# Kernel tuning notes

Measured on AMD Instinct MI355X. Metric: run time of the kernel, lower is better.

The kernel has to match this reference:

```python
import jax, jax.numpy as jnp
import numpy as np

B, S, D = 2, 2048, 2048
NH, NKV, HD = 16, 4, 128
EPS = 1e-6


def rmsnorm(x, w, eps=EPS):
    # torch.nn.RMSNorm: x * rsqrt(mean(x^2) + eps) * weight
    ms = jnp.mean(jnp.square(x), axis=-1, keepdims=True)
    return x * jax.lax.rsqrt(ms + eps) * w


def apply_rotary_emb(x, freqs_cis):
    # x: (B, S, H, HD); freqs_cis: (S, HD//2, 2) -> pairwise complex rotation (gpt-fast style)
    xs = x.reshape(*x.shape[:-1], -1, 2)          # (B,S,H,HD//2,2)
    fc = freqs_cis[None, :, None, :, :]           # (1,S,1,HD//2,2)
    xr, xi = xs[..., 0], xs[..., 1]
    fr, fi = fc[..., 0], fc[..., 1]
    out = jnp.stack([xr * fr - xi * fi, xi * fr + xr * fi], axis=-1)
    return out.reshape(x.shape)


def setup_inputs() -> dict:
    key = jax.random.key(0)
    ks = jax.random.split(key, 4)
    x = jax.random.normal(ks[0], (B, S, D), dtype=jnp.float32)
    freqs_cis = jax.random.normal(ks[1], (S, HD // 2, 2), dtype=jnp.float32)
    wqkv = jax.random.normal(ks[2], ((NH + 2 * NKV) * HD, D), dtype=jnp.float32) * (D ** -0.5)
    wo = jax.random.normal(ks[3], (NH * HD, D), dtype=jnp.float32).T * ((NH * HD) ** -0.5)
    wo = jnp.asarray(wo)  # (D, NH*HD) torch layout (out,in)
    q_norm_w = jnp.ones((HD,), dtype=jnp.float32)
    k_norm_w = jnp.ones((HD,), dtype=jnp.float32)
    return {"x": x, "freqs_cis": freqs_cis, "wqkv": wqkv, "wo": wo,
            "q_norm_w": q_norm_w, "k_norm_w": k_norm_w}


def reference(x, freqs_cis, wqkv, wo, q_norm_w, k_norm_w):
    b, s, _ = x.shape
    q_size, kv_size = NH * HD, NKV * HD
    qkv = jnp.einsum('bsd,ed->bse', x, wqkv)  # fused QKV projection
    q, k, v = jnp.split(qkv, [q_size, q_size + kv_size], axis=-1)
    q = q.reshape(b, s, NH, HD)
    k = k.reshape(b, s, NKV, HD)
    v = v.reshape(b, s, NKV, HD)
    q = rmsnorm(q, q_norm_w)
    k = rmsnorm(k, k_norm_w)
    q = apply_rotary_emb(q, freqs_cis)
    k = apply_rotary_emb(k, freqs_cis)
    # GQA: repeat_interleave KV heads to NH
    rep = NH // NKV
    k = jnp.repeat(k, rep, axis=2)  # (b,s,NH,HD)
    v = jnp.repeat(v, rep, axis=2)
    scale = 1.0 / np.sqrt(HD)
    scores = jnp.einsum('bqhd,bkhd->bhqk', q, k) * scale
    causal = jnp.tril(jnp.ones((s, s), dtype=bool))
    scores = jnp.where(causal[None, None], scores, -jnp.inf)
    attn = jax.nn.softmax(scores, axis=-1)
    y = jnp.einsum('bhqk,bkhd->bqhd', attn, v)
    y = y.reshape(b, s, q_size)
    return jnp.einsum('bse,de->bsd', y, wo)
```

## Files before the change

### kernel.cpp

```cpp
#include <hip/hip_runtime.h>
#include <math.h>

constexpr int B_ = 2, S_ = 2048, D_ = 2048, NH_ = 16, NKV_ = 4, HD_ = 128;
constexpr int EQKV_ = (NH_ + 2 * NKV_) * HD_;
constexpr int M_ = B_ * S_;
constexpr float EPS_ = 1e-6f;
constexpr float QSCALE_ = 0.08838834764831845f;

typedef __attribute__((ext_vector_type(8))) short bf16x8;
typedef __attribute__((ext_vector_type(4))) float f32x4;
typedef __attribute__((address_space(1))) unsigned int gu32;
typedef __attribute__((address_space(3))) unsigned int lu32;

__device__ inline ushort f2bf(float f) {
    unsigned u = __float_as_uint(f);
    return (ushort)((u + 0x7FFF + ((u >> 16) & 1)) >> 16);
}

constexpr int NP_X = M_ * D_ / 4;
constexpr int NP_W = EQKV_ * D_ / 4;
constexpr int NP_O = D_ * NH_ * HD_ / 4;
__global__ __launch_bounds__(256) void pack_all(
    const float* __restrict__ x, const float* __restrict__ wqkv,
    const float* __restrict__ wo,
    ushort* __restrict__ xbf, ushort* __restrict__ wqkvbf,
    ushort* __restrict__ wobf)
{
    int i = blockIdx.x * 256 + threadIdx.x;
    const float4* src; ushort4* dst; int j;
    if (i < NP_X)                 { src = (const float4*)x;    dst = (ushort4*)xbf;    j = i; }
    else if (i < NP_X + NP_W)     { src = (const float4*)wqkv; dst = (ushort4*)wqkvbf; j = i - NP_X; }
    else if (i < NP_X + NP_W + NP_O) { src = (const float4*)wo; dst = (ushort4*)wobf;  j = i - NP_X - NP_W; }
    else return;
    float4 f = src[j];
    ushort4 u;
    u.x = f2bf(f.x); u.y = f2bf(f.y); u.z = f2bf(f.z); u.w = f2bf(f.w);
    dst[j] = u;
}

__global__ __launch_bounds__(256) void gemm_nt_bf16(
    const ushort* __restrict__ A, const ushort* __restrict__ W,
    float* __restrict__ C, int M, int N, int K)
{
    __shared__ __align__(16) ushort As[128 * 64];
    __shared__ __align__(16) ushort Bs[128 * 64];
    const int t = threadIdx.x;
    const int wave = t >> 6, lane = t & 63;
    const int nwg = gridDim.x * gridDim.y;
    int wg = blockIdx.y * gridDim.x + blockIdx.x;
    wg = (wg & 7) * (nwg >> 3) + (wg >> 3);
    const int m0 = (wg / gridDim.x) * 128, n0 = (wg % gridDim.x) * 128;
    const int wm = (wave >> 1) * 64, wn = (wave & 1) * 64;
    const int lrow = lane & 15, lquad = lane >> 4;

    const int srow = t >> 3;
    const int sgo = ((t & 7) ^ (srow & 7)) * 8;
    const ushort* Aa = A + (size_t)(m0 + srow) * K + sgo;
    const ushort* Wa = W + (size_t)(n0 + srow) * K + sgo;
    const int rs0 = (lquad ^ (lrow & 7)) * 8;
    const int rs1 = rs0 ^ 32;

    f32x4 acc[4][4];
#pragma unroll
    for (int i = 0; i < 4; ++i)
#pragma unroll
        for (int j = 0; j < 4; ++j) acc[i][j] = (f32x4){0.f, 0.f, 0.f, 0.f};

    for (int k0 = 0; k0 < K; k0 += 64) {
        __syncthreads();
#pragma unroll
        for (int i = 0; i < 4; ++i) {
            const int ub = (wave * 64 + 256 * i) * 8;
            __builtin_amdgcn_global_load_lds(
                (const gu32*)(Aa + (size_t)(32 * i) * K + k0),
                (lu32*)(As + ub), 16, 0, 0);
            __builtin_amdgcn_global_load_lds(
                (const gu32*)(Wa + (size_t)(32 * i) * K + k0),
                (lu32*)(Bs + ub), 16, 0, 0);
        }
        __syncthreads();

#pragma unroll
        for (int ks = 0; ks < 2; ++ks) {
            const int so = ks ? rs1 : rs0;
            bf16x8 af[4], bf[4];
#pragma unroll
            for (int i = 0; i < 4; ++i) {
                af[i] = *(const bf16x8*)(As + (wm + i * 16 + lrow) * 64 + so);
                bf[i] = *(const bf16x8*)(Bs + (wn + i * 16 + lrow) * 64 + so);
            }
#pragma unroll
            for (int i = 0; i < 4; ++i)
#pragma unroll
                for (int j = 0; j < 4; ++j)
                    acc[i][j] = __builtin_amdgcn_mfma_f32_16x16x32_bf16(
                        af[i], bf[j], acc[i][j], 0, 0, 0);
        }
    }
#pragma unroll
    for (int i = 0; i < 4; ++i)
#pragma unroll
        for (int j = 0; j < 4; ++j) {
            float* cp = C + (size_t)(m0 + wm + i * 16 + lquad * 4) * N
                          + n0 + wn + j * 16 + lrow;
#pragma unroll
            for (int r = 0; r < 4; ++r) cp[(size_t)r * N] = acc[i][j][r];
        }
}

__global__ __launch_bounds__(256) void gemm_qkv_fused(
    const ushort* __restrict__ A,
    const ushort* __restrict__ W,
    const float* __restrict__ freqs,
    const float* __restrict__ qw, const float* __restrict__ kw,
    ushort* __restrict__ qo, ushort* __restrict__ ko, ushort* __restrict__ vo,
    int K)
{
    __shared__ __align__(16) ushort smem[128 * 136];
    __shared__ float rsbuf[256];
    ushort* As = smem;
    ushort* Bs = smem + 4096;
    ushort* Lt = smem;

    const int t = threadIdx.x;
    const int wave = t >> 6, lane = t & 63;
    const int nwg = gridDim.x * gridDim.y;
    int wg = blockIdx.y * gridDim.x + blockIdx.x;
    wg = (wg & 7) * (nwg >> 3) + (wg >> 3);
    const int m0 = (wg / gridDim.x) * 128, n0 = (wg % gridDim.x) * 128;
    const int wm = (wave >> 1) * 64, wn = (wave & 1) * 64;
    const int half = wave & 1;
    const int lrow = lane & 15, lquad = lane >> 4;
    const int head = n0 >> 7;
    const int b = m0 >> 11, s0 = m0 & (S_ - 1);

    f32x4 acc[4][4];
#pragma unroll
    for (int i = 0; i < 4; ++i)
#pragma unroll
        for (int j = 0; j < 4; ++j) acc[i][j] = (f32x4){0.f, 0.f, 0.f, 0.f};

    for (int k0 = 0; k0 < K; k0 += 32) {
        __syncthreads();
#pragma unroll
        for (int i = 0; i < 2; ++i) {
            int chunk = t + 256 * i;
            int row = chunk >> 2, seg = chunk & 3;
            int ubase = (wave * 64 + 256 * i) * 8;
            __builtin_amdgcn_global_load_lds(
                (const gu32*)(A + (size_t)(m0 + row) * K + k0 + seg * 8),
                (lu32*)(As + ubase), 16, 0, 0);
            __builtin_amdgcn_global_load_lds(
                (const gu32*)(W + (size_t)(n0 + row) * K + k0 + seg * 8),
                (lu32*)(Bs + ubase), 16, 0, 0);
        }
        __syncthreads();

        bf16x8 af[4], bf[4];
#pragma unroll
        for (int i = 0; i < 4; ++i) {
            af[i] = *(const bf16x8*)(As + (wm + i * 16 + lrow) * 32 + lquad * 8);
            bf[i] = *(const bf16x8*)(Bs + (wn + i * 16 + lrow) * 32 + lquad * 8);
        }
#pragma unroll
        for (int i = 0; i < 4; ++i)
#pragma unroll
            for (int j = 0; j < 4; ++j)
                acc[i][j] = __builtin_amdgcn_mfma_f32_16x16x32_bf16(
                    af[i], bf[j], acc[i][j], 0, 0, 0);
    }
    __syncthreads();

    float part[4][4];
    if (head < NH_ + NKV_) {
#pragma unroll
        for (int i = 0; i < 4; ++i)
#pragma unroll
            for (int r = 0; r < 4; ++r) {
                float p = acc[i][0][r] * acc[i][0][r]
                        + acc[i][1][r] * acc[i][1][r]
                        + acc[i][2][r] * acc[i][2][r]
                        + acc[i][3][r] * acc[i][3][r];
#pragma unroll
                for (int off = 1; off < 16; off <<= 1) p += __shfl_xor(p, off);
                part[i][r] = p;
                if (lrow == 0)
                    rsbuf[half * 128 + wm + i * 16 + lquad * 4 + r] = p;
            }
    }
    __syncthreads();

    if (head < NH_ + NKV_) {
        const float* nw = (head < NH_) ? qw : kw;
        float wv[4];
#pragma unroll
        for (int j = 0; j < 4; ++j) wv[j] = nw[wn + j * 16 + lrow];
#pragma unroll
        for (int i = 0; i < 4; ++i)
#pragma unroll
            for (int r = 0; r < 4; ++r) {
                const int rowid = wm + i * 16 + lquad * 4 + r;
                const int s = s0 + rowid;
                const float total = part[i][r] + rsbuf[(half ^ 1) * 128 + rowid];
                const float rs = rsqrtf(total * (1.0f / HD_) + EPS_);
#pragma unroll
                for (int j = 0; j < 4; ++j) {
                    const int d = wn + j * 16 + lrow;
                    const float xn = acc[i][j][r] * rs * wv[j];
                    const float other = __shfl_xor(xn, 1);
                    const float fr = freqs[s * HD_ + (d & ~1)];
                    const float fi = freqs[s * HD_ + (d & ~1) + 1];
                    float out = (d & 1) ? fmaf(xn, fr, other * fi)
                                        : fmaf(xn, fr, -other * fi);
                    if (head < NH_) out *= QSCALE_;
                    Lt[rowid * 136 + d] = f2bf(out);
                }
            }
    } else {
#pragma unroll
        for (int i = 0; i < 4; ++i)
#pragma unroll
            for (int j = 0; j < 4; ++j)
#pragma unroll
                for (int r = 0; r < 4; ++r)
                    Lt[(wn + j * 16 + lrow) * 136 + wm + i * 16 + lquad * 4 + r]
                        = f2bf(acc[i][j][r]);
    }
    __syncthreads();

    const int g = t >> 4, lx16 = t & 15;
    if (head < NH_) {
        ushort* dst0 = qo + ((size_t)(b * NH_ + head) * S_ + s0) * HD_;
#pragma unroll
        for (int it = 0; it < 8; ++it) {
            const int rowid = it * 16 + g;
            uint4 v = *(const uint4*)(Lt + rowid * 136 + lx16 * 8);
            *(uint4*)(dst0 + (size_t)rowid * HD_ + lx16 * 8) = v;
        }
    } else if (head < NH_ + NKV_) {
        const int kh = head - NH_;
        ushort* dst0 = ko + ((size_t)(b * NKV_ + kh) * S_ + s0) * HD_;
#pragma unroll
        for (int it = 0; it < 8; ++it) {
            const int rowid = it * 16 + g;
            uint4 v = *(const uint4*)(Lt + rowid * 136 + lx16 * 8);
            *(uint4*)(dst0 + (size_t)rowid * HD_ + lx16 * 8) = v;
        }
    } else {
        const int vh = head - (NH_ + NKV_);
        ushort* dst0 = vo + ((size_t)(b * NKV_ + vh) * HD_) * S_ + s0;
#pragma unroll
        for (int it = 0; it < 8; ++it) {
            const int rowid = it * 16 + g;
            uint4 v = *(const uint4*)(Lt + rowid * 136 + lx16 * 8);
            *(uint4*)(dst0 + (size_t)rowid * S_ + lx16 * 8) = v;
        }
    }
}

__global__ __launch_bounds__(512, 4) void flash_attn_mfma(
    const ushort* __restrict__ Q,
    const ushort* __restrict__ K,
    const ushort* __restrict__ V,
    ushort* __restrict__ Y,
    float* __restrict__ OP,
    float* __restrict__ ML)
{
    __shared__ __align__(16) ushort Ks[4 * 64 * 32];
    __shared__ __align__(16) ushort Vs[2 * 128 * 32];
    __shared__ __align__(16) ushort Ps[8 * 16 * 72];

    const int t = threadIdx.x, w = t >> 6, lane = t & 63;
    const int lx = lane & 15, quad = lane >> 4;
    const int h = blockIdx.y, b = blockIdx.z;

    const int gx = blockIdx.x;
    int qb, halfsel, tk0, tk1;
    bool split;
    if (gx < 22) {
        split = true;
        qb = 15 - (gx >> 1);
        halfsel = gx & 1;
        const int h0 = qb + 1;
        tk0 = halfsel ? h0 : 0;
        tk1 = halfsel ? 2 * qb + 2 : h0;
    } else {
        split = false;
        qb = 26 - gx;
        halfsel = 0;
        tk0 = 0;
        tk1 = 2 * qb + 2;
    }
    const int q0 = qb * 128;
    const int kvh = h >> 2;

    const int srow8 = lane >> 3, sseg8 = lane & 7;
    const int fsw = (srow8 >> 1) & 3;
    const int slotw = ((sseg8 & 3) ^ fsw) * 8;
    const int krow = w * 8 + srow8;
    const int d0 = w * 8 + srow8;
    ushort* kdst = Ks + (sseg8 >> 2) * 2048 + krow * 32 + slotw;
    ushort* vdst = Vs + (sseg8 >> 2) * 4096 + d0 * 32 + slotw;
    const ushort* ksrc = K + ((size_t)(b * NKV_ + kvh) * S_ + krow) * HD_
                           + sseg8 * 8;
    const ushort* vsrc = V + ((size_t)(b * NKV_ + kvh) * HD_ + d0) * S_
                           + sseg8 * 8;
    const int rslot = (quad ^ ((lx >> 1) & 3)) * 8;

    const ushort* qb_ = Q + ((size_t)(b * NH_ + h) * S_ + q0) * HD_;
    bf16x8 aq[4];
#pragma unroll
    for (int ks = 0; ks < 4; ++ks)
        aq[ks] = *(const bf16x8*)(qb_ + (size_t)(w * 16 + lx) * HD_ + ks * 32 + quad * 8);

    f32x4 o[8];
#pragma unroll
    for (int j = 0; j < 8; ++j) o[j] = (f32x4){0.f, 0.f, 0.f, 0.f};
    float mrow[4] = {-INFINITY, -INFINITY, -INFINITY, -INFINITY};
    float lp[4] = {0.f, 0.f, 0.f, 0.f};

    uint4 kr0, kr1, vr0, vr1;
    {
        const size_t kf = (size_t)tk0 * 64;
        kr0 = *(const uint4*)(ksrc + kf * HD_);
        kr1 = *(const uint4*)(ksrc + kf * HD_ + 64);
        vr0 = *(const uint4*)(vsrc + kf);
        vr1 = *(const uint4*)(vsrc + (size_t)64 * S_ + kf);
    }

    for (int tk = tk0; tk < tk1; ++tk) {
        const int k0 = tk * 64;
        asm volatile("s_barrier" ::: "memory");
        *(uint4*)(kdst +    0) = kr0;
        *(uint4*)(kdst + 4096) = kr1;
        *(uint4*)(vdst +    0) = vr0;
        *(uint4*)(vdst + 2048) = vr1;
        asm volatile("s_waitcnt lgkmcnt(0)" ::: "memory");
        asm volatile("s_barrier" ::: "memory");

        if (tk + 1 < tk1) {
            const size_t kf = (size_t)(k0 + 64);
            kr0 = *(const uint4*)(ksrc + kf * HD_);
            kr1 = *(const uint4*)(ksrc + kf * HD_ + 64);
            vr0 = *(const uint4*)(vsrc + kf);
            vr1 = *(const uint4*)(vsrc + (size_t)64 * S_ + kf);
        }

        f32x4 s[4];
#pragma unroll
        for (int j = 0; j < 4; ++j) s[j] = (f32x4){0.f, 0.f, 0.f, 0.f};
        __builtin_amdgcn_s_setprio(1);
#pragma unroll
        for (int ks = 0; ks < 4; ++ks) {
#pragma unroll
            for (int j = 0; j < 4; ++j) {
                bf16x8 bk = *(const bf16x8*)(Ks + ks * 2048 + (j * 16 + lx) * 32 + rslot);
                s[j] = __builtin_amdgcn_mfma_f32_16x16x32_bf16(aq[ks], bk, s[j], 0, 0, 0);
            }
        }
        __builtin_amdgcn_s_setprio(0);

        const int qrow_base = q0 + w * 16 + quad * 4;
        if (k0 + 63 > q0 + w * 16) {
#pragma unroll
            for (int reg = 0; reg < 4; ++reg) {
                const int qrow = qrow_base + reg;
#pragma unroll
                for (int j = 0; j < 4; ++j)
                    if (k0 + lx + 16 * j > qrow) s[j][reg] = -INFINITY;
            }
        }

        float rmx[4];
        bool need = false;
#pragma unroll
        for (int reg = 0; reg < 4; ++reg) {
            rmx[reg] = fmaxf(fmaxf(s[0][reg], s[1][reg]),
                             fmaxf(s[2][reg], s[3][reg]));
            need |= (rmx[reg] > mrow[reg] + 8.0f);
        }
        if (__any(need)) {
#pragma unroll
            for (int reg = 0; reg < 4; ++reg) {
                float rm = rmx[reg];
#pragma unroll
                for (int off = 1; off < 16; off <<= 1)
                    rm = fmaxf(rm, __shfl_xor(rm, off));
                const float mn = fmaxf(mrow[reg], rm);
                const float alpha = __expf(mrow[reg] - mn);
                mrow[reg] = mn;
                lp[reg] *= alpha;
#pragma unroll
                for (int j = 0; j < 8; ++j) o[j][reg] *= alpha;
            }
        }
#pragma unroll
        for (int reg = 0; reg < 4; ++reg) {
#pragma unroll
            for (int j = 0; j < 4; ++j) {
                const float p = __expf(s[j][reg] - mrow[reg]);
                lp[reg] += p;
                Ps[w * 1152 + (quad * 4 + reg) * 72 + lx + 16 * j] = f2bf(p);
            }
        }

        bf16x8 ap[2];
#pragma unroll
        for (int ks2 = 0; ks2 < 2; ++ks2)
            ap[ks2] = *(const bf16x8*)(Ps + w * 1152 + lx * 72 + ks2 * 32 + quad * 8);
        __builtin_amdgcn_s_setprio(1);
#pragma unroll
        for (int jd = 0; jd < 8; ++jd) {
#pragma unroll
            for (int ks2 = 0; ks2 < 2; ++ks2) {
                bf16x8 bv = *(const bf16x8*)(Vs + ks2 * 4096 + (jd * 16 + lx) * 32 + rslot);
                o[jd] = __builtin_amdgcn_mfma_f32_16x16x32_bf16(ap[ks2], bv, o[jd], 0, 0, 0);
            }
        }
        __builtin_amdgcn_s_setprio(0);
    }

#pragma unroll
    for (int reg = 0; reg < 4; ++reg) {
        float l = lp[reg];
#pragma unroll
        for (int off = 1; off < 16; off <<= 1) l += __shfl_xor(l, off);
        lp[reg] = l;
    }
    if (!split) {
#pragma unroll
        for (int reg = 0; reg < 4; ++reg) {
            const float inv = 1.0f / lp[reg];
            const size_t yb = (size_t)(b * S_ + q0 + w * 16 + quad * 4 + reg) * (NH_ * HD_)
                            + h * HD_ + lx;
#pragma unroll
            for (int jd = 0; jd < 8; ++jd)
                Y[yb + jd * 16] = f2bf(o[jd][reg] * inv);
        }
    } else {
        const int sp = ((b * NH_ + h) * 11 + (qb - 5)) * 2 + halfsel;
        float* mlb = ML + (size_t)sp * 256;
#pragma unroll
        for (int reg = 0; reg < 4; ++reg) {
            const int row = w * 16 + quad * 4 + reg;
            if (lx == 0) {
                mlb[row] = mrow[reg];
                mlb[128 + row] = lp[reg];
            }
            float* ob = OP + ((size_t)sp * 128 + row) * 128 + lx;
#pragma unroll
            for (int jd = 0; jd < 8; ++jd)
                ob[jd * 16] = o[jd][reg];
        }
    }
}

__global__ __launch_bounds__(256) void attn_combine(
    const float* __restrict__ OP, const float* __restrict__ ML,
    ushort* __restrict__ Y)
{
    const int gx = blockIdx.x, h = blockIdx.y, b = blockIdx.z;
    const int qb = 5 + gx;
    const int q0 = qb * 128;
    const int sp0 = ((b * NH_ + h) * 11 + gx) * 2;
    const float* ml0 = ML + (size_t)sp0 * 256;
    const float* ml1 = ML + (size_t)(sp0 + 1) * 256;
    const float* o0 = OP + (size_t)sp0 * 128 * 128;
    const float* o1 = OP + (size_t)(sp0 + 1) * 128 * 128;
    const int d = threadIdx.x & 127, rg = threadIdx.x >> 7;
#pragma unroll
    for (int r = rg; r < 128; r += 2) {
        const float m0 = ml0[r], l0 = ml0[128 + r];
        const float m1 = ml1[r], l1 = ml1[128 + r];
        const float m = fmaxf(m0, m1);
        const float w0 = __expf(m0 - m), w1 = __expf(m1 - m);
        const float inv = 1.0f / (l0 * w0 + l1 * w1);
        const float v = (o0[r * 128 + d] * w0 + o1[r * 128 + d] * w1) * inv;
        Y[((size_t)(b * S_ + q0 + r)) * (NH_ * HD_) + h * HD_ + d] = f2bf(v);
    }
}

extern "C" void kernel_launch(void* const* d_in, const int* in_sizes, int n_in,
                              void* d_out, int out_size, void* d_ws, size_t ws_size,
                              hipStream_t stream)
{
    const float* x     = (const float*)d_in[0];
    const float* freqs = (const float*)d_in[1];
    const float* wqkv  = (const float*)d_in[2];
    const float* wo    = (const float*)d_in[3];
    const float* qw    = (const float*)d_in[4];
    const float* kw    = (const float*)d_in[5];
    float* out = (float*)d_out;

    char* ws = (char*)d_ws;
    ushort* qbf    = (ushort*)(ws + 0);
    ushort* kbf    = (ushort*)(ws + 16777216);
    ushort* vtb    = (ushort*)(ws + 20971520);
    ushort* ybf    = (ushort*)(ws + 25165824);
    ushort* wobf   = (ushort*)(ws + 41943040);
    ushort* wqkvbf = (ushort*)(ws + 50331648);
    ushort* xbf    = (ushort*)(ws + 83886080);
    float*  OP     = (float*)(ws + 50331648);
    float*  ML     = (float*)(ws + 96468992);

    pack_all<<<(NP_X + NP_W + NP_O + 255) / 256, 256, 0, stream>>>(
        x, wqkv, wo, xbf, wqkvbf, wobf);
    gemm_qkv_fused<<<dim3(EQKV_ / 128, M_ / 128), 256, 0, stream>>>(
        xbf, wqkvbf, freqs, qw, kw, qbf, kbf, vtb, D_);
    flash_attn_mfma<<<dim3(27, NH_, B_), 512, 0, stream>>>(qbf, kbf, vtb, ybf,
                                                           OP, ML);
    attn_combine<<<dim3(11, NH_, B_), 256, 0, stream>>>(OP, ML, ybf);
    gemm_nt_bf16<<<dim3(D_ / 128, M_ / 128), 256, 0, stream>>>(
        ybf, wobf, out, M_, D_, NH_ * HD_);
}
```

Measured before the change: 335.9 us.

## Split QKV GEMM K-dimension across two wave groups with in-block reduction

```diff
diff --git a/kernel.cpp b/kernel.cpp
--- a/kernel.cpp
+++ b/kernel.cpp
@@ -108,7 +108,7 @@
         }
 }
 
-__global__ __launch_bounds__(256) void gemm_qkv_fused(
+__global__ __launch_bounds__(512, 4) void gemm_qkv_fused(
     const ushort* __restrict__ A,
     const ushort* __restrict__ W,
     const float* __restrict__ freqs,
@@ -116,51 +116,57 @@
     ushort* __restrict__ qo, ushort* __restrict__ ko, ushort* __restrict__ vo,
     int K)
 {
-    __shared__ __align__(16) ushort smem[128 * 136];
+    __shared__ __align__(16) ushort smem[17408];
     __shared__ float rsbuf[256];
-    ushort* As = smem;
-    ushort* Bs = smem + 4096;
     ushort* Lt = smem;
+    float* red = (float*)smem;
 
     const int t = threadIdx.x;
     const int wave = t >> 6, lane = t & 63;
+    const int grp = wave >> 2;
+    const int wl = wave & 3;
+    const int tl = t & 255;
     const int nwg = gridDim.x * gridDim.y;
     int wg = blockIdx.y * gridDim.x + blockIdx.x;
     wg = (wg & 7) * (nwg >> 3) + (wg >> 3);
     const int m0 = (wg / gridDim.x) * 128, n0 = (wg % gridDim.x) * 128;
-    const int wm = (wave >> 1) * 64, wn = (wave & 1) * 64;
-    const int half = wave & 1;
+    const int wm = (wl >> 1) * 64, wn = (wl & 1) * 64;
+    const int half = wl & 1;
     const int lrow = lane & 15, lquad = lane >> 4;
     const int head = n0 >> 7;
     const int b = m0 >> 11, s0 = m0 & (S_ - 1);
 
+    ushort* Ag = smem + grp * 4096;
+    ushort* Bg = smem + 8192 + grp * 4096;
+    const int kbase = grp * 1024;
+
     f32x4 acc[4][4];
 #pragma unroll
     for (int i = 0; i < 4; ++i)
 #pragma unroll
         for (int j = 0; j < 4; ++j) acc[i][j] = (f32x4){0.f, 0.f, 0.f, 0.f};
 
-    for (int k0 = 0; k0 < K; k0 += 32) {
+    for (int k0 = 0; k0 < 1024; k0 += 32) {
         __syncthreads();
 #pragma unroll
         for (int i = 0; i < 2; ++i) {
-            int chunk = t + 256 * i;
+            int chunk = tl + 256 * i;
             int row = chunk >> 2, seg = chunk & 3;
-            int ubase = (wave * 64 + 256 * i) * 8;
+            int ubase = (wl * 64 + 256 * i) * 8;
             __builtin_amdgcn_global_load_lds(
-                (const gu32*)(A + (size_t)(m0 + row) * K + k0 + seg * 8),
-                (lu32*)(As + ubase), 16, 0, 0);
+                (const gu32*)(A + (size_t)(m0 + row) * K + kbase + k0 + seg * 8),
+                (lu32*)(Ag + ubase), 16, 0, 0);
             __builtin_amdgcn_global_load_lds(
-                (const gu32*)(W + (size_t)(n0 + row) * K + k0 + seg * 8),
-                (lu32*)(Bs + ubase), 16, 0, 0);
+                (const gu32*)(W + (size_t)(n0 + row) * K + kbase + k0 + seg * 8),
+                (lu32*)(Bg + ubase), 16, 0, 0);
         }
         __syncthreads();
 
         bf16x8 af[4], bf[4];
 #pragma unroll
         for (int i = 0; i < 4; ++i) {
-            af[i] = *(const bf16x8*)(As + (wm + i * 16 + lrow) * 32 + lquad * 8);
-            bf[i] = *(const bf16x8*)(Bs + (wn + i * 16 + lrow) * 32 + lquad * 8);
+            af[i] = *(const bf16x8*)(Ag + (wm + i * 16 + lrow) * 32 + lquad * 8);
+            bf[i] = *(const bf16x8*)(Bg + (wn + i * 16 + lrow) * 32 + lquad * 8);
         }
 #pragma unroll
         for (int i = 0; i < 4; ++i)
@@ -169,10 +175,36 @@
                 acc[i][j] = __builtin_amdgcn_mfma_f32_16x16x32_bf16(
                     af[i], bf[j], acc[i][j], 0, 0, 0);
     }
+
     __syncthreads();
+#pragma unroll
+    for (int c = 0; c < 2; ++c) {
+        if (grp == 1 && half == c) {
+#pragma unroll
+            for (int i = 0; i < 4; ++i)
+#pragma unroll
+                for (int j = 0; j < 4; ++j)
+#pragma unroll
+                    for (int r = 0; r < 4; ++r)
+                        red[(wm + i * 16 + lquad * 4 + r) * 65 + j * 16 + lrow]
+                            = acc[i][j][r];
+        }
+        __syncthreads();
+        if (grp == 0 && half == c) {
+#pragma unroll
+            for (int i = 0; i < 4; ++i)
+#pragma unroll
+                for (int j = 0; j < 4; ++j)
+#pragma unroll
+                    for (int r = 0; r < 4; ++r)
+                        acc[i][j][r] +=
+                            red[(wm + i * 16 + lquad * 4 + r) * 65 + j * 16 + lrow];
+        }
+        __syncthreads();
+    }
 
     float part[4][4];
-    if (head < NH_ + NKV_) {
+    if (grp == 0 && head < NH_ + NKV_) {
 #pragma unroll
         for (int i = 0; i < 4; ++i)
 #pragma unroll
@@ -190,41 +222,43 @@
     }
     __syncthreads();
 
-    if (head < NH_ + NKV_) {
-        const float* nw = (head < NH_) ? qw : kw;
-        float wv[4];
-#pragma unroll
-        for (int j = 0; j < 4; ++j) wv[j] = nw[wn + j * 16 + lrow];
-#pragma unroll
-        for (int i = 0; i < 4; ++i)
-#pragma unroll
-            for (int r = 0; r < 4; ++r) {
-                const int rowid = wm + i * 16 + lquad * 4 + r;
-                const int s = s0 + rowid;
-                const float total = part[i][r] + rsbuf[(half ^ 1) * 128 + rowid];
-                const float rs = rsqrtf(total * (1.0f / HD_) + EPS_);
-#pragma unroll
-                for (int j = 0; j < 4; ++j) {
-                    const int d = wn + j * 16 + lrow;
-                    const float xn = acc[i][j][r] * rs * wv[j];
-                    const float other = __shfl_xor(xn, 1);
-                    const float fr = freqs[s * HD_ + (d & ~1)];
-                    const float fi = freqs[s * HD_ + (d & ~1) + 1];
-                    float out = (d & 1) ? fmaf(xn, fr, other * fi)
-                                        : fmaf(xn, fr, -other * fi);
-                    if (head < NH_) out *= QSCALE_;
-                    Lt[rowid * 136 + d] = f2bf(out);
+    if (grp == 0) {
+        if (head < NH_ + NKV_) {
+            const float* nw = (head < NH_) ? qw : kw;
+            float wv[4];
+#pragma unroll
+            for (int j = 0; j < 4; ++j) wv[j] = nw[wn + j * 16 + lrow];
+#pragma unroll
+            for (int i = 0; i < 4; ++i)
+#pragma unroll
+                for (int r = 0; r < 4; ++r) {
+                    const int rowid = wm + i * 16 + lquad * 4 + r;
+                    const int s = s0 + rowid;
+                    const float total = part[i][r] + rsbuf[(half ^ 1) * 128 + rowid];
+                    const float rs = rsqrtf(total * (1.0f / HD_) + EPS_);
+#pragma unroll
+                    for (int j = 0; j < 4; ++j) {
+                        const int d = wn + j * 16 + lrow;
+                        const float xn = acc[i][j][r] * rs * wv[j];
+                        const float other = __shfl_xor(xn, 1);
+                        const float fr = freqs[s * HD_ + (d & ~1)];
+                        const float fi = freqs[s * HD_ + (d & ~1) + 1];
+                        float out = (d & 1) ? fmaf(xn, fr, other * fi)
+                                            : fmaf(xn, fr, -other * fi);
+                        if (head < NH_) out *= QSCALE_;
+                        Lt[rowid * 136 + d] = f2bf(out);
+                    }
                 }
-            }
-    } else {
-#pragma unroll
-        for (int i = 0; i < 4; ++i)
-#pragma unroll
-            for (int j = 0; j < 4; ++j)
-#pragma unroll
-                for (int r = 0; r < 4; ++r)
-                    Lt[(wn + j * 16 + lrow) * 136 + wm + i * 16 + lquad * 4 + r]
-                        = f2bf(acc[i][j][r]);
+        } else {
+#pragma unroll
+            for (int i = 0; i < 4; ++i)
+#pragma unroll
+                for (int j = 0; j < 4; ++j)
+#pragma unroll
+                    for (int r = 0; r < 4; ++r)
+                        Lt[(wn + j * 16 + lrow) * 136 + wm + i * 16 + lquad * 4 + r]
+                            = f2bf(acc[i][j][r]);
+        }
     }
     __syncthreads();
 
@@ -232,8 +266,8 @@
     if (head < NH_) {
         ushort* dst0 = qo + ((size_t)(b * NH_ + head) * S_ + s0) * HD_;
 #pragma unroll
-        for (int it = 0; it < 8; ++it) {
-            const int rowid = it * 16 + g;
+        for (int it = 0; it < 4; ++it) {
+            const int rowid = it * 32 + g;
             uint4 v = *(const uint4*)(Lt + rowid * 136 + lx16 * 8);
             *(uint4*)(dst0 + (size_t)rowid * HD_ + lx16 * 8) = v;
         }
@@ -241,8 +275,8 @@
         const int kh = head - NH_;
         ushort* dst0 = ko + ((size_t)(b * NKV_ + kh) * S_ + s0) * HD_;
 #pragma unroll
-        for (int it = 0; it < 8; ++it) {
-            const int rowid = it * 16 + g;
+        for (int it = 0; it < 4; ++it) {
+            const int rowid = it * 32 + g;
             uint4 v = *(const uint4*)(Lt + rowid * 136 + lx16 * 8);
             *(uint4*)(dst0 + (size_t)rowid * HD_ + lx16 * 8) = v;
         }
@@ -250,8 +284,8 @@
         const int vh = head - (NH_ + NKV_);
         ushort* dst0 = vo + ((size_t)(b * NKV_ + vh) * HD_) * S_ + s0;
 #pragma unroll
-        for (int it = 0; it < 8; ++it) {
-            const int rowid = it * 16 + g;
+        for (int it = 0; it < 4; ++it) {
+            const int rowid = it * 32 + g;
             uint4 v = *(const uint4*)(Lt + rowid * 136 + lx16 * 8);
             *(uint4*)(dst0 + (size_t)rowid * S_ + lx16 * 8) = v;
         }
@@ -505,7 +539,7 @@
 
     pack_all<<<(NP_X + NP_W + NP_O + 255) / 256, 256, 0, stream>>>(
         x, wqkv, wo, xbf, wqkvbf, wobf);
-    gemm_qkv_fused<<<dim3(EQKV_ / 128, M_ / 128), 256, 0, stream>>>(
+    gemm_qkv_fused<<<dim3(EQKV_ / 128, M_ / 128), 512, 0, stream>>>(
         xbf, wqkvbf, freqs, qw, kw, qbf, kbf, vtb, D_);
     flash_attn_mfma<<<dim3(27, NH_, B_), 512, 0, stream>>>(qbf, kbf, vtb, ybf,
                                                            OP, ML);
```

After: 347.9 us. 1.04x slower.
